# Kernel tuning notes

Measured on AMD Instinct MI355X. Metric: run time of the kernel, lower is better.

## Reference

```python
import jax, jax.numpy as jnp
import numpy as np

TP, TQ, B = 600, 60, 64          # passage len, question len, batch
H, H2, EMB = 256, 128, 344       # hidden, hidden//2, embed(300)+pos_tags(44)


def _lstm_cell(x, h, c, Wih, Whh, b):
    # PyTorch nn.LSTMCell math; b = b_ih + b_hh, gate order i,f,g,o
    g = x @ Wih.T + h @ Whh.T + b
    i, f, gg, o = jnp.split(g, 4, axis=-1)
    c2 = jax.nn.sigmoid(f) * c + jax.nn.sigmoid(i) * jnp.tanh(gg)
    return jax.nn.sigmoid(o) * jnp.tanh(c2), c2


def _pre_bilstm(x, mask, Wih, Whh, b):
    # Faithful quirk of the source: the cell's h output is DISCARDED;
    # c is masked and h = tanh(c).
    Bb = x.shape[1]
    init = (jnp.zeros((Bb, H2), x.dtype), jnp.zeros((Bb, H2), x.dtype))

    def step(carry, inp):
        h, c = carry
        xt, mt = inp
        _, c2 = _lstm_cell(xt, h, c, Wih, Whh, b)
        c2 = c2 * mt
        h2 = jnp.tanh(c2)
        return (h2, c2), h2

    _, Hf = jax.lax.scan(step, init, (x, mask))
    _, Hb = jax.lax.scan(step, init, (x[::-1], mask[::-1]))
    return jnp.concatenate([Hf, Hb[::-1]], axis=-1)  # [T,B,H]


def _match(Hp, Hq, mask, Wq, Wp, bp, Wh, Wa, ba, Wih, Whh, b):
    aq = Hq @ Wq.T           # [TQ,B,H] attend_question_for_passage (no bias)
    ap = Hp @ Wp.T + bp      # [TP,B,H] attend_passage_for_passage (precomputed)
    Bb = Hp.shape[1]
    init = (jnp.zeros((Bb, H2), Hp.dtype), jnp.zeros((Bb, H2), Hp.dtype))

    def step(carry, inp):
        h, c = carry
        apt, hpt, mt = inp
        g = jnp.tanh(aq + apt + h @ Wh.T)               # [TQ,B,H]
        alpha = jax.nn.softmax(g @ Wa.T + ba, axis=0)   # softmax over TQ, [TQ,B,1]
        wHq = jnp.einsum('tbo,tbh->bh', alpha, Hq)      # weighted question
        z = jnp.concatenate([hpt, wHq], axis=-1)        # [B,2H]
        h2, c2 = _lstm_cell(z, h, c, Wih, Whh, b)
        h2, c2 = h2 * mt, c2 * mt                       # mask applied to h and c
        return (h2, c2), h2

    _, Hf = jax.lax.scan(step, init, (ap, Hp, mask))
    _, Hb = jax.lax.scan(step, init, (ap[::-1], Hp[::-1], mask[::-1]))
    return jnp.concatenate([Hf, Hb[::-1]], axis=-1)  # [TP,B,H]


def setup_inputs() -> dict:
    key = jax.random.key(0)
    ks = iter(jax.random.split(key, 32))

    def w(shape, s=0.08):
        return jax.random.normal(next(ks), shape, jnp.float32) * s

    return {
        "passage": jax.random.normal(next(ks), (TP, B, EMB), jnp.float32),
        "question": jax.random.normal(next(ks), (TQ, B, EMB), jnp.float32),
        "mask_p": jnp.ones((TP, B, 1), jnp.float32),
        "mask_q": jnp.ones((TQ, B, 1), jnp.float32),
        "pre0_Wih": w((4 * H2, EMB)), "pre0_Whh": w((4 * H2, H2)), "pre0_b": w((4 * H2,)),
        "pre1_Wih": w((4 * H2, H)), "pre1_Whh": w((4 * H2, H2)), "pre1_b": w((4 * H2,)),
        "mq_Wq": w((H, H)), "mq_Wp": w((H, H)), "mq_bp": w((H,)),
        "mq_Wh": w((H, H2)), "mq_Wa": w((1, H)), "mq_ba": w((1,)),
        "mq_Wih": w((4 * H2, 2 * H)), "mq_Whh": w((4 * H2, H2)), "mq_b": w((4 * H2,)),
    }


def reference(passage, question, mask_p, mask_q,
              pre0_Wih, pre0_Whh, pre0_b,
              pre1_Wih, pre1_Whh, pre1_b,
              mq_Wq, mq_Wp, mq_bp, mq_Wh, mq_Wa, mq_ba,
              mq_Wih, mq_Whh, mq_b):
    # preprocessing layer 0 (shared LSTM for passage and question), dropout=0 eval
    Hp = _pre_bilstm(passage, mask_p, pre0_Wih, pre0_Whh, pre0_b)
    Hq = _pre_bilstm(question, mask_q, pre0_Wih, pre0_Whh, pre0_b)
    # preprocessing layer 1
    Hp = _pre_bilstm(Hp, mask_p, pre1_Wih, pre1_Whh, pre1_b)
    Hq = _pre_bilstm(Hq, mask_q, pre1_Wih, pre1_Whh, pre1_b)
    # passage Match-LSTM layer (bidirectional, question-attention per step)
    Hr = _match(Hp, Hq, mask_p, mq_Wq, mq_Wp, mq_bp, mq_Wh, mq_Wa, mq_ba,
                mq_Wih, mq_Whh, mq_b)
    return Hr  # [TP, B, H]
```

## Files before the change

### kernel.cpp

```cpp
#include <hip/hip_runtime.h>

typedef unsigned int u32;
typedef _Float16 f16x2 __attribute__((ext_vector_type(2)));

#define TP 600
#define TQ 60
#define BB 64
#define EMB 344
#define HH 256
#define H2 128
#define GG 512

__device__ __forceinline__ float exp2_fast(float x){
#if __has_builtin(__builtin_amdgcn_exp2f)
    return __builtin_amdgcn_exp2f(x);
#else
    return exp2f(x);
#endif
}
__device__ __forceinline__ float rcp_fast(float x){
#if __has_builtin(__builtin_amdgcn_rcpf)
    return __builtin_amdgcn_rcpf(x);
#else
    return 1.0f / x;
#endif
}
__device__ __forceinline__ float sigm_fast(float x){
    return rcp_fast(1.f + exp2_fast(-1.44269504f * x));
}
__device__ __forceinline__ float tanh_fast(float x){
    return 1.f - 2.f * rcp_fast(1.f + exp2_fast(2.88539008f * x));
}
__device__ __forceinline__ float dot2x(u32 w, u32 h, float acc){
    f16x2 wv = __builtin_bit_cast(f16x2, w);
    f16x2 hv = __builtin_bit_cast(f16x2, h);
    acc = fmaf((float)wv.x, (float)hv.x, acc);
    acc = fmaf((float)wv.y, (float)hv.y, acc);
    return acc;
}
__device__ __forceinline__ float dot2f(u32 w, u32 h, float acc){
#if __has_builtin(__builtin_amdgcn_fdot2)
    return __builtin_amdgcn_fdot2(__builtin_bit_cast(f16x2, w),
                                  __builtin_bit_cast(f16x2, h), acc, false);
#else
    return dot2x(w, h, acc);
#endif
}
__device__ __forceinline__ u32 pack2(float a, float b){
    f16x2 v; v.x = (_Float16)a; v.y = (_Float16)b;
    return __builtin_bit_cast(u32, v);
}
__device__ __forceinline__ u32 lane_bcast(u32 v, int l){
    return (u32)__builtin_amdgcn_readlane((int)v, l);
}
__device__ __forceinline__ void bar_lds(){
    asm volatile("s_waitcnt lgkmcnt(0)\n\ts_barrier" ::: "memory");
}

__global__ void prep_kernel(const float* __restrict__ pre0_Wih, const float* __restrict__ pre0_Whh,
                            const float* __restrict__ pre1_Wih, const float* __restrict__ pre1_Whh,
                            const float* __restrict__ Wq, const float* __restrict__ Wp,
                            const float* __restrict__ Whm,
                            const float* __restrict__ Whhm,
                            float* __restrict__ WT0, float* __restrict__ WT1,
                            float* __restrict__ WTq, float* __restrict__ WTp,
                            float* __restrict__ WTz, const float* __restrict__ Wihm,
                            u32* __restrict__ P0hh, u32* __restrict__ P1hh,
                            u32* __restrict__ PMhh, u32* __restrict__ PMwh)
{
    int g = blockIdx.x * blockDim.x + threadIdx.x;
    int gs = gridDim.x * blockDim.x;
    for (int idx = g; idx < 512*344; idx += gs) {
        int j = idx / 344, k = idx - j*344;
        WT0[((k>>2)*512 + j)*4 + (k&3)] = pre0_Wih[idx];
    }
    for (int idx = g; idx < 512*256; idx += gs) {
        int j = idx >> 8, k = idx & 255;
        WT1[((k>>2)*512 + j)*4 + (k&3)] = pre1_Wih[idx];
    }
    for (int idx = g; idx < 256*256; idx += gs) {
        int j = idx >> 8, k = idx & 255;
        WTq[((k>>2)*256 + j)*4 + (k&3)] = Wq[idx];
        WTp[((k>>2)*256 + j)*4 + (k&3)] = Wp[idx];
    }
    for (int idx = g; idx < 512*256; idx += gs) {
        int j = idx >> 8, k = idx & 255;
        WTz[((k>>2)*512 + j)*4 + (k&3)] = Wihm[j*512 + k];
    }
    for (int idx = g; idx < 64*512; idx += gs) {
        int k2 = idx >> 9, j = idx & 511;
        P0hh[idx] = pack2(pre0_Whh[j*128 + 2*k2], pre0_Whh[j*128 + 2*k2 + 1]);
        P1hh[idx] = pack2(pre1_Whh[j*128 + 2*k2], pre1_Whh[j*128 + 2*k2 + 1]);
        PMhh[idx] = pack2(Whhm[j*128 + 2*k2], Whhm[j*128 + 2*k2 + 1]);
    }
    for (int idx = g; idx < 64*256; idx += gs) {
        int k2 = idx >> 8, j = idx & 255;
        PMwh[idx] = pack2(Whm[j*128 + 2*k2], Whm[j*128 + 2*k2 + 1]);
    }
}

template<int K, int M>
__global__ __launch_bounds__(M)
void proj_kernel(const float* __restrict__ X0, const float* __restrict__ W0,
                 const float* __restrict__ b0, float* __restrict__ C0, int T0,
                 const float* __restrict__ X1, const float* __restrict__ W1,
                 const float* __restrict__ b1, float* __restrict__ C1)
{
    __shared__ float Xs[K*68];
    int t = blockIdx.x;
    const float* X; const float* W; const float* bias; float* C; int trow;
    if (t < T0) { X = X0; W = W0; bias = b0; C = C0; trow = t; }
    else        { X = X1; W = W1; bias = b1; C = C1; trow = t - T0; }
    int j = threadIdx.x;
    for (int b = 0; b < 64; ++b) {
        for (int k = j; k < K; k += M)
            Xs[k*68 + b] = X[(trow*64 + b)*K + k];
    }
    __syncthreads();
    float acc[64];
    float binit = bias ? bias[j] : 0.f;
    #pragma unroll
    for (int b = 0; b < 64; ++b) acc[b] = binit;
    const float4* W4 = (const float4*)W;
    for (int k4 = 0; k4 < K/4; ++k4) {
        float4 w4 = W4[k4*M + j];
        float wv[4] = {w4.x, w4.y, w4.z, w4.w};
        #pragma unroll
        for (int kk = 0; kk < 4; ++kk) {
            int k = 4*k4 + kk;
            #pragma unroll
            for (int b4 = 0; b4 < 16; ++b4) {
                float4 x4 = *((const float4*)&Xs[k*68 + 4*b4]);
                acc[4*b4+0] = fmaf(wv[kk], x4.x, acc[4*b4+0]);
                acc[4*b4+1] = fmaf(wv[kk], x4.y, acc[4*b4+1]);
                acc[4*b4+2] = fmaf(wv[kk], x4.z, acc[4*b4+2]);
                acc[4*b4+3] = fmaf(wv[kk], x4.w, acc[4*b4+3]);
            }
        }
    }
    for (int b = 0; b < 64; ++b)
        C[(trow*64 + b)*M + j] = acc[b];
}

__global__ __launch_bounds__(512)
void yq_kernel(const float* __restrict__ Hq1, const float* __restrict__ Wihm,
               float* __restrict__ Yq)
{
    __shared__ float Xs[256*68];
    int tq = blockIdx.x;
    int j = threadIdx.x;
    for (int b = 0; b < 64; ++b) {
        for (int k = j; k < 256; k += 512)
            Xs[k*68 + b] = Hq1[(tq*64 + b)*256 + k];
    }
    __syncthreads();
    float acc[64];
    #pragma unroll
    for (int b = 0; b < 64; ++b) acc[b] = 0.f;
    const float4* W4 = (const float4*)(Wihm + j*512 + 256);
    for (int k4 = 0; k4 < 64; ++k4) {
        float4 w4 = W4[k4];
        float wv[4] = {w4.x, w4.y, w4.z, w4.w};
        #pragma unroll
        for (int kk = 0; kk < 4; ++kk) {
            int k = 4*k4 + kk;
            #pragma unroll
            for (int b4 = 0; b4 < 16; ++b4) {
                float4 x4 = *((const float4*)&Xs[k*68 + 4*b4]);
                acc[4*b4+0] = fmaf(wv[kk], x4.x, acc[4*b4+0]);
                acc[4*b4+1] = fmaf(wv[kk], x4.y, acc[4*b4+1]);
                acc[4*b4+2] = fmaf(wv[kk], x4.z, acc[4*b4+2]);
                acc[4*b4+3] = fmaf(wv[kk], x4.w, acc[4*b4+3]);
            }
        }
    }
    for (int b = 0; b < 64; ++b)
        Yq[(tq*64 + b)*512 + j] = acc[b];
}

__global__ __launch_bounds__(128)
__attribute__((amdgpu_waves_per_eu(1, 1)))
void rec_pre_kernel(const float* __restrict__ Xp, const float* __restrict__ Xq,
                    const u32* __restrict__ Whh,
                    const float* __restrict__ mask_p, const float* __restrict__ mask_q,
                    float* __restrict__ Hp, float* __restrict__ Hq)
{
    int bid = blockIdx.x;
    int sub = bid & 127; int b = sub >> 1; int dir = sub & 1;
    const float* X; const float* mask; float* Hout; int T;
    if (bid < 128) { X = Xp; mask = mask_p; Hout = Hp; T = TP; }
    else           { X = Xq; mask = mask_q; Hout = Hq; T = TQ; }
    int j = threadIdx.x;
    int l = j & 63;
    __shared__ __align__(8) _Float16 hbuf[2][128];
    u32 wi[64], wf[64], wg[64];
    #pragma unroll
    for (int q = 0; q < 64; ++q) {
        wi[q] = Whh[q*512 +       j];
        wf[q] = Whh[q*512 + 128 + j];
        wg[q] = Whh[q*512 + 256 + j];
    }
    hbuf[0][j] = (_Float16)0.f;
    float c = 0.f;
    int t0 = dir ? (T-1) : 0;
    int t1i = (T > 1) ? (dir ? (T-2) : 1) : t0;
    float xi0 = X[(t0*64+b)*512 + j],       xf0 = X[(t0*64+b)*512 + 128 + j],
          xg0 = X[(t0*64+b)*512 + 256 + j], m0  = mask[t0*64+b];
    float xi1 = X[(t1i*64+b)*512 + j],       xf1 = X[(t1i*64+b)*512 + 128 + j],
          xg1 = X[(t1i*64+b)*512 + 256 + j], m1  = mask[t1i*64+b];
    bar_lds();
    int buf = 0;
    const u32* hb32 = (const u32*)hbuf;
    for (int s = 0; s < T; ++s) {
        int ti = dir ? (T-1-s) : s;
        int s2 = (s+2 < T) ? (s+2) : (T-1);
        int t2 = dir ? (T-1-s2) : s2;
        float xi2 = X[(t2*64+b)*512 + j],       xf2 = X[(t2*64+b)*512 + 128 + j],
              xg2 = X[(t2*64+b)*512 + 256 + j], m2  = mask[t2*64+b];
        u32 hp = hb32[buf*64 + l];
        float ai0 = xi0, ai1 = 0.f, af0 = xf0, af1 = 0.f, ag0 = xg0, ag1 = 0.f;
        #pragma unroll
        for (int q = 0; q < 64; q += 2) {
            u32 h0 = lane_bcast(hp, q), h1 = lane_bcast(hp, q+1);
            ai0 = dot2f(wi[q],   h0, ai0); af0 = dot2f(wf[q],   h0, af0); ag0 = dot2f(wg[q],   h0, ag0);
            ai1 = dot2f(wi[q+1], h1, ai1); af1 = dot2f(wf[q+1], h1, af1); ag1 = dot2f(wg[q+1], h1, ag1);
        }
        float gi = sigm_fast(ai0 + ai1);
        float gf = sigm_fast(af0 + af1);
        float gg = tanh_fast(ag0 + ag1);
        c = gf*c + gi*gg;
        c *= m0;
        float h = tanh_fast(c);
        hbuf[buf^1][j] = (_Float16)h;
        Hout[(ti*64 + b)*256 + dir*128 + j] = h;
        bar_lds();
        buf ^= 1;
        xi0=xi1; xf0=xf1; xg0=xg1; m0=m1;
        xi1=xi2; xf1=xf2; xg1=xg2; m1=m2;
    }
}

__global__ __launch_bounds__(512)
__attribute__((amdgpu_waves_per_eu(2, 2)))
void match_kernel(const float* __restrict__ ap,
                  const float* __restrict__ aqg,
                  const float* __restrict__ Zp,
                  const float* __restrict__ Yq,
                  const float* __restrict__ Wa,
                  const float* __restrict__ mask_p,
                  const u32* __restrict__ PMwh,
                  const u32* __restrict__ PMhh,
                  float* __restrict__ out)
{
    int bid = blockIdx.x; int b = bid >> 1; int dir = bid & 1;
    int tid = threadIdx.x;
    __shared__ __align__(16) u32 sumt16[160];
    __shared__ __align__(16) float gates[512];
    __shared__ __align__(16) _Float16 e16[64];

    int tq = tid >> 3, sb = tid & 7, l = tid & 63;

    u32 aqr[16];
    if (tq < 60) {
        #pragma unroll
        for (int i = 0; i < 16; ++i) {
            float2 a = *(const float2*)&aqg[(tq*64 + b)*256 + 32*sb + 2*i];
            aqr[i] = pack2(a.x, a.y);
        }
    } else {
        #pragma unroll
        for (int i = 0; i < 16; ++i) aqr[i] = 0u;
    }
    u32 wa_reg[16];
    #pragma unroll
    for (int i = 0; i < 16; ++i) {
        float2 w2 = *(const float2*)&Wa[32*sb + 2*i];
        wa_reg[i] = pack2(w2.x, w2.y);
    }
    u32 Yqr[32];
    #pragma unroll
    for (int r = 0; r < 30; ++r) {
        float y0 = Yq[((2*r  )*64 + b)*512 + tid];
        float y1 = Yq[((2*r+1)*64 + b)*512 + tid];
        Yqr[r] = pack2(y0, y1);
    }
    Yqr[30] = 0u; Yqr[31] = 0u;
    u32 whh[64];
    #pragma unroll
    for (int q = 0; q < 64; ++q) whh[q] = PMhh[q*512 + tid];
    u32 wh[64];
    {
        int jw = tid & 255;
        #pragma unroll
        for (int q = 0; q < 64; ++q) wh[q] = PMwh[q*256 + jw];
    }

    float c0 = 0.f, c1 = 0.f;
    u32 hp = 0u;
    int ti0 = dir ? (TP-1) : 0;
    float zp_c = Zp[(ti0*64 + b)*512 + tid];
    float ap_c = (tid < 256) ? ap[(ti0*64 + b)*256 + tid] : 0.f;
    float m_c  = mask_p[ti0*64 + b];
    int cls = tid >> 7;
    const u32 ONE2 = 0x3C003C00u;
    float h_out0 = 0.f, h_out1 = 0.f; int ti_prev = 0;
    bar_lds();

    const u32* e32 = (const u32*)e16;

    for (int s = 0; s < TP; ++s) {
        int ti = dir ? (TP-1-s) : s;
        int s1 = (s+1 < TP) ? (s+1) : s;
        int tn = dir ? (TP-1-s1) : s1;

        float w0 = 0.f, w1 = 0.f, w2a = 0.f, w3a = 0.f;
        if (tid < 256) {
            float s0 = ap_c, s1a = 0.f, s2 = 0.f, s3 = 0.f;
            #pragma unroll
            for (int q = 0; q < 64; q += 4) {
                u32 h0 = lane_bcast(hp, q),   u1 = lane_bcast(hp, q+1);
                u32 h2v = lane_bcast(hp, q+2), h3 = lane_bcast(hp, q+3);
                w0  = dot2f(whh[q],   h0,  w0);  s0  = dot2f(wh[q],   h0,  s0);
                w1  = dot2f(whh[q+1], u1,  w1);  s1a = dot2f(wh[q+1], u1,  s1a);
                w2a = dot2f(whh[q+2], h2v, w2a); s2  = dot2f(wh[q+2], h2v, s2);
                w3a = dot2f(whh[q+3], h3,  w3a); s3  = dot2f(wh[q+3], h3,  s3);
            }
            float st = (s0 + s1a) + (s2 + s3);
            float so = __shfl_xor(st, 1);
            if ((tid & 1) == 0) {
                int p = tid >> 1;
                sumt16[(p >> 4)*20 + (p & 15)] = pack2(st, so);
            }
        } else {
            #pragma unroll
            for (int q = 0; q < 64; q += 4) {
                u32 h0 = lane_bcast(hp, q),   u1 = lane_bcast(hp, q+1);
                u32 h2v = lane_bcast(hp, q+2), h3 = lane_bcast(hp, q+3);
                w0  = dot2f(whh[q],   h0,  w0);
                w1  = dot2f(whh[q+1], u1,  w1);
                w2a = dot2f(whh[q+2], h2v, w2a);
                w3a = dot2f(whh[q+3], h3,  w3a);
            }
        }
        float hwhh = (w0 + w1) + (w2a + w3a);
        bar_lds();

        if (s && tid < 64) {
            float2 hv; hv.x = h_out0; hv.y = h_out1;
            *(float2*)&out[(ti_prev*64 + b)*256 + dir*128 + 2*l] = hv;
        }
        float zp_n = Zp[(tn*64 + b)*512 + tid];
        float ap_n = (tid < 256) ? ap[(tn*64 + b)*256 + tid] : 0.f;
        float m_n  = mask_p[tn*64 + b];

        {
            const uint4* sv4 = (const uint4*)&sumt16[sb*20];
            uint4 sv0 = sv4[0], sv1 = sv4[1], sv2 = sv4[2], sv3 = sv4[3];
            u32 sa[16] = {sv0.x,sv0.y,sv0.z,sv0.w, sv1.x,sv1.y,sv1.z,sv1.w,
                          sv2.x,sv2.y,sv2.z,sv2.w, sv3.x,sv3.y,sv3.z,sv3.w};
            float p0 = 0.f, p1 = 0.f, p2 = 0.f, p3 = 0.f;
            #pragma unroll
            for (int i = 0; i < 16; ++i) {
                f16x2 sm = __builtin_bit_cast(f16x2, aqr[i]) +
                           __builtin_bit_cast(f16x2, sa[i]);
                f16x2 wv = __builtin_bit_cast(f16x2, wa_reg[i]);
                float t0 = tanh_fast((float)sm.x);
                float t1 = tanh_fast((float)sm.y);
                if (i & 1) { p2 = fmaf((float)wv.x, t0, p2); p3 = fmaf((float)wv.y, t1, p3); }
                else       { p0 = fmaf((float)wv.x, t0, p0); p1 = fmaf((float)wv.y, t1, p1); }
            }
            float part = (p0 + p1) + (p2 + p3);
            part += __shfl_xor(part, 1);
            part += __shfl_xor(part, 2);
            part += __shfl_xor(part, 4);
            float sc = fminf(9.f, fmaxf(-9.f, part));
            float e = exp2_fast(sc * 1.44269504f);
            if (tq >= 60) e = 0.f;
            if (sb == 0) e16[tq] = (_Float16)e;
        }
        bar_lds();

        {
            u32 ep = e32[l & 31];
            float y0 = 0.f, y1 = 0.f, S0 = 0.f, S1 = 0.f;
            #pragma unroll
            for (int r4 = 0; r4 < 8; ++r4) {
                u32 e0 = lane_bcast(ep, 4*r4+0), e1 = lane_bcast(ep, 4*r4+1);
                u32 e2 = lane_bcast(ep, 4*r4+2), e3 = lane_bcast(ep, 4*r4+3);
                y0 = dot2f(Yqr[4*r4+0], e0, y0); S0 = dot2f(ONE2, e0, S0);
                y1 = dot2f(Yqr[4*r4+1], e1, y1); S1 = dot2f(ONE2, e1, S1);
                y0 = dot2f(Yqr[4*r4+2], e2, y0); S0 = dot2f(ONE2, e2, S0);
                y1 = dot2f(Yqr[4*r4+3], e3, y1); S1 = dot2f(ONE2, e3, S1);
            }
            float rn = rcp_fast(S0 + S1);
            float g = zp_c + rn * (y0 + y1) + hwhh;
            gates[tid] = (cls == 2) ? tanh_fast(g) : sigm_fast(g);
        }
        bar_lds();

        {
            float2 gi2 = *(const float2*)&gates[      2*l];
            float2 gf2 = *(const float2*)&gates[128 + 2*l];
            float2 gg2 = *(const float2*)&gates[256 + 2*l];
            float2 go2 = *(const float2*)&gates[384 + 2*l];
            c0 = gf2.x*c0 + gi2.x*gg2.x;
            c1 = gf2.y*c1 + gi2.y*gg2.y;
            float h0 = go2.x * tanh_fast(c0);
            float h1 = go2.y * tanh_fast(c1);
            h0 *= m_c; h1 *= m_c; c0 *= m_c; c1 *= m_c;
            hp = pack2(h0, h1);
            h_out0 = h0; h_out1 = h1; ti_prev = ti;
        }
        zp_c = zp_n; ap_c = ap_n; m_c = m_n;
    }
    if (tid < 64) {
        float2 hv; hv.x = h_out0; hv.y = h_out1;
        *(float2*)&out[(ti_prev*64 + b)*256 + dir*128 + 2*l] = hv;
    }
}

#define O_BUFX   0UL
#define O_BUFXQ  19660800UL
#define O_HP0    21626880UL
#define O_HQ0    31457280UL
#define O_HP1    32440320UL
#define O_HQ1    42270720UL
#define O_WT0    43253760UL
#define O_WT1    43429888UL
#define O_WTQ    43560960UL
#define O_WTP    43626496UL
#define O_WTZ    43692032UL
#define O_P0HH   43823104UL
#define O_P1HH   43855872UL
#define O_PMHH   43888640UL
#define O_PMWH   43921408UL

extern "C" void kernel_launch(void* const* d_in, const int* in_sizes, int n_in,
                              void* d_out, int out_size, void* d_ws, size_t ws_size,
                              hipStream_t stream)
{
    const float* passage  = (const float*)d_in[0];
    const float* question = (const float*)d_in[1];
    const float* mask_p   = (const float*)d_in[2];
    const float* mask_q   = (const float*)d_in[3];
    const float* pre0_Wih = (const float*)d_in[4];
    const float* pre0_Whh = (const float*)d_in[5];
    const float* pre0_b   = (const float*)d_in[6];
    const float* pre1_Wih = (const float*)d_in[7];
    const float* pre1_Whh = (const float*)d_in[8];
    const float* pre1_b   = (const float*)d_in[9];
    const float* mq_Wq    = (const float*)d_in[10];
    const float* mq_Wp    = (const float*)d_in[11];
    const float* mq_bp    = (const float*)d_in[12];
    const float* mq_Wh    = (const float*)d_in[13];
    const float* mq_Wa    = (const float*)d_in[14];
    const float* mq_Wih   = (const float*)d_in[16];
    const float* mq_Whh   = (const float*)d_in[17];
    const float* mq_b     = (const float*)d_in[18];

    float* ws = (float*)d_ws;
    float* bufX  = ws + O_BUFX;
    float* bufXq = ws + O_BUFXQ;
    float* Hp0   = ws + O_HP0;
    float* Hq0   = ws + O_HQ0;
    float* Hp1   = ws + O_HP1;
    float* Hq1   = ws + O_HQ1;
    float* WT0   = ws + O_WT0;
    float* WT1   = ws + O_WT1;
    float* WTq   = ws + O_WTQ;
    float* WTp   = ws + O_WTP;
    float* WTz   = ws + O_WTZ;
    u32*   P0hh  = (u32*)(ws + O_P0HH);
    u32*   P1hh  = (u32*)(ws + O_P1HH);
    u32*   PMhh  = (u32*)(ws + O_PMHH);
    u32*   PMwh  = (u32*)(ws + O_PMWH);
    float* ap = Hp0;
    float* aq = Hq0;
    float* Zp = bufX;
    float* Yq = bufXq;

    prep_kernel<<<688, 256, 0, stream>>>(pre0_Wih, pre0_Whh, pre1_Wih, pre1_Whh,
                                         mq_Wq, mq_Wp, mq_Wh, mq_Whh,
                                         WT0, WT1, WTq, WTp, WTz, mq_Wih,
                                         P0hh, P1hh, PMhh, PMwh);
    proj_kernel<EMB, 512><<<660, 512, 0, stream>>>(passage, WT0, pre0_b, bufX, TP,
                                                   question, WT0, pre0_b, bufXq);
    rec_pre_kernel<<<256, 128, 0, stream>>>(bufX, bufXq, P0hh, mask_p, mask_q, Hp0, Hq0);
    proj_kernel<256, 512><<<660, 512, 0, stream>>>(Hp0, WT1, pre1_b, bufX, TP,
                                                   Hq0, WT1, pre1_b, bufXq);
    rec_pre_kernel<<<256, 128, 0, stream>>>(bufX, bufXq, P1hh, mask_p, mask_q, Hp1, Hq1);
    proj_kernel<256, 256><<<660, 256, 0, stream>>>(Hp1, WTp, mq_bp, ap, TP,
                                                   Hq1, WTq, nullptr, aq);
    proj_kernel<256, 512><<<600, 512, 0, stream>>>(Hp1, WTz, mq_b, Zp, TP,
                                                   nullptr, nullptr, nullptr, nullptr);
    yq_kernel<<<60, 512, 0, stream>>>(Hq1, mq_Wih, Yq);
    match_kernel<<<128, 512, 0, stream>>>(ap, aq, Zp, Yq, mq_Wa, mask_p,
                                          PMwh, PMhh, (float*)d_out);
}
```

Before: 3.820 ms.

## Split recurrent matvecs across more waves with warp-specialized partial sums

The pre-LSTM recurrence now uses 768 threads per block instead of 128. Six waves each compute half of the hidden-state dot product for the three gates, and a second group supplies the other half through shared memory. The match kernel grows to 1024 threads: one half computes the Whh gate matvec and the other computes the attention Wh projection. Both halves split the attention score and weighted-question reductions, and the partial results are combined in LDS. The aim is to shorten the serial per-step critical path by spreading register-resident weights and FLOPs over more waves, at the cost of extra barriers and LDS traffic per step.

```diff
diff --git a/kernel.cpp b/kernel.cpp
--- a/kernel.cpp
+++ b/kernel.cpp
@@ -55,6 +55,46 @@
 }
 __device__ __forceinline__ void bar_lds(){
     asm volatile("s_waitcnt lgkmcnt(0)\n\ts_barrier" ::: "memory");
+}
+
+__device__ __forceinline__ void attn_p2(int tq2, int sub, const u32* aqr,
+                                        const float* sumt_s, const float* wa_s,
+                                        _Float16* e16)
+{
+    float p0 = 0.f, p1 = 0.f;
+    #pragma unroll
+    for (int i = 0; i < 8; ++i) {
+        f16x2 av = __builtin_bit_cast(f16x2, aqr[i]);
+        float2 st = *(const float2*)&sumt_s[16*sub + 2*i];
+        float2 wv = *(const float2*)&wa_s[16*sub + 2*i];
+        p0 = fmaf(wv.x, tanh_fast((float)av.x + st.x), p0);
+        p1 = fmaf(wv.y, tanh_fast((float)av.y + st.y), p1);
+    }
+    float part = p0 + p1;
+    part += __shfl_xor(part, 1);
+    part += __shfl_xor(part, 2);
+    part += __shfl_xor(part, 4);
+    part += __shfl_xor(part, 8);
+    if (sub == 0 && tq2 < 60) {
+        float sc = fminf(9.f, fmaxf(-9.f, part));
+        e16[tq2] = (_Float16)exp2_fast(sc * 1.44269504f);
+    }
+}
+__device__ __forceinline__ void cell4(const float* gates, int l, float m,
+                                      float& c0, float& c1, u32& hp,
+                                      float& h0o, float& h1o)
+{
+    float2 gi2 = *(const float2*)&gates[      2*l];
+    float2 gf2 = *(const float2*)&gates[128 + 2*l];
+    float2 gg2 = *(const float2*)&gates[256 + 2*l];
+    float2 go2 = *(const float2*)&gates[384 + 2*l];
+    c0 = gf2.x*c0 + gi2.x*gg2.x;
+    c1 = gf2.y*c1 + gi2.y*gg2.y;
+    float h0 = go2.x * tanh_fast(c0);
+    float h1 = go2.y * tanh_fast(c1);
+    h0 *= m; h1 *= m; c0 *= m; c1 *= m;
+    hp = pack2(h0, h1);
+    h0o = h0; h1o = h1;
 }
 
 __global__ void prep_kernel(const float* __restrict__ pre0_Wih, const float* __restrict__ pre0_Whh,
@@ -178,70 +218,99 @@
         Yq[(tq*64 + b)*512 + j] = acc[b];
 }
 
-__global__ __launch_bounds__(128)
-__attribute__((amdgpu_waves_per_eu(1, 1)))
+__global__ __launch_bounds__(768)
 void rec_pre_kernel(const float* __restrict__ Xp, const float* __restrict__ Xq,
                     const u32* __restrict__ Whh,
                     const float* __restrict__ mask_p, const float* __restrict__ mask_q,
                     float* __restrict__ Hp, float* __restrict__ Hq)
 {
     int bid = blockIdx.x;
-    int sub = bid & 127; int b = sub >> 1; int dir = sub & 1;
+    int sb2 = bid & 127; int b = sb2 >> 1; int dir = sb2 & 1;
     const float* X; const float* mask; float* Hout; int T;
     if (bid < 128) { X = Xp; mask = mask_p; Hout = Hp; T = TP; }
     else           { X = Xq; mask = mask_q; Hout = Hq; T = TQ; }
-    int j = threadIdx.x;
-    int l = j & 63;
-    __shared__ __align__(8) _Float16 hbuf[2][128];
-    u32 wi[64], wf[64], wg[64];
-    #pragma unroll
-    for (int q = 0; q < 64; ++q) {
-        wi[q] = Whh[q*512 +       j];
-        wf[q] = Whh[q*512 + 128 + j];
-        wg[q] = Whh[q*512 + 256 + j];
-    }
-    hbuf[0][j] = (_Float16)0.f;
-    float c = 0.f;
+    int t = threadIdx.x;
+    int l = t & 63;
+    __shared__ float gates[384];
+    __shared__ float partG[384];
+    u32 hp = 0u;
+    float c0 = 0.f, c1 = 0.f;
     int t0 = dir ? (T-1) : 0;
     int t1i = (T > 1) ? (dir ? (T-2) : 1) : t0;
-    float xi0 = X[(t0*64+b)*512 + j],       xf0 = X[(t0*64+b)*512 + 128 + j],
-          xg0 = X[(t0*64+b)*512 + 256 + j], m0  = mask[t0*64+b];
-    float xi1 = X[(t1i*64+b)*512 + j],       xf1 = X[(t1i*64+b)*512 + 128 + j],
-          xg1 = X[(t1i*64+b)*512 + 256 + j], m1  = mask[t1i*64+b];
-    bar_lds();
-    int buf = 0;
-    const u32* hb32 = (const u32*)hbuf;
-    for (int s = 0; s < T; ++s) {
-        int ti = dir ? (T-1-s) : s;
-        int s2 = (s+2 < T) ? (s+2) : (T-1);
-        int t2 = dir ? (T-1-s2) : s2;
-        float xi2 = X[(t2*64+b)*512 + j],       xf2 = X[(t2*64+b)*512 + 128 + j],
-              xg2 = X[(t2*64+b)*512 + 256 + j], m2  = mask[t2*64+b];
-        u32 hp = hb32[buf*64 + l];
-        float ai0 = xi0, ai1 = 0.f, af0 = xf0, af1 = 0.f, ag0 = xg0, ag1 = 0.f;
-        #pragma unroll
-        for (int q = 0; q < 64; q += 2) {
-            u32 h0 = lane_bcast(hp, q), h1 = lane_bcast(hp, q+1);
-            ai0 = dot2f(wi[q],   h0, ai0); af0 = dot2f(wf[q],   h0, af0); ag0 = dot2f(wg[q],   h0, ag0);
-            ai1 = dot2f(wi[q+1], h1, ai1); af1 = dot2f(wf[q+1], h1, af1); ag1 = dot2f(wg[q+1], h1, ag1);
-        }
-        float gi = sigm_fast(ai0 + ai1);
-        float gf = sigm_fast(af0 + af1);
-        float gg = tanh_fast(ag0 + ag1);
-        c = gf*c + gi*gg;
-        c *= m0;
-        float h = tanh_fast(c);
-        hbuf[buf^1][j] = (_Float16)h;
-        Hout[(ti*64 + b)*256 + dir*128 + j] = h;
-        bar_lds();
-        buf ^= 1;
-        xi0=xi1; xf0=xf1; xg0=xg1; m0=m1;
-        xi1=xi2; xf1=xf2; xg1=xg2; m1=m2;
-    }
-}
-
-__global__ __launch_bounds__(512)
-__attribute__((amdgpu_waves_per_eu(2, 2)))
+    float m_c = mask[t0*64 + b];
+    float m_1 = mask[t1i*64 + b];
+
+    if (t < 384) {
+        int j = t;
+        u32 w[32];
+        #pragma unroll
+        for (int q = 0; q < 32; ++q) w[q] = Whh[q*512 + j];
+        float x_c = X[(t0*64 + b)*512 + j];
+        float x_1 = X[(t1i*64 + b)*512 + j];
+        float hd0, hd1;
+        for (int s = 0; s < T; ++s) {
+            int ti = dir ? (T-1-s) : s;
+            int s2 = (s+2 < T) ? (s+2) : (T-1);
+            int t2 = dir ? (T-1-s2) : s2;
+            float x_2 = X[(t2*64 + b)*512 + j];
+            float m_2 = mask[t2*64 + b];
+            float a0 = 0.f, a1 = 0.f;
+            #pragma unroll
+            for (int q = 0; q < 32; q += 2) {
+                a0 = dot2f(w[q],   lane_bcast(hp, q),   a0);
+                a1 = dot2f(w[q+1], lane_bcast(hp, q+1), a1);
+            }
+            bar_lds();
+            float g = x_c + (a0 + a1) + partG[j];
+            gates[j] = ((j >> 7) == 2) ? tanh_fast(g) : sigm_fast(g);
+            bar_lds();
+            {
+                float2 gi2 = *(const float2*)&gates[      2*l];
+                float2 gf2 = *(const float2*)&gates[128 + 2*l];
+                float2 gg2 = *(const float2*)&gates[256 + 2*l];
+                c0 = gf2.x*c0 + gi2.x*gg2.x;  c0 *= m_c;
+                c1 = gf2.y*c1 + gi2.y*gg2.y;  c1 *= m_c;
+                hd0 = tanh_fast(c0); hd1 = tanh_fast(c1);
+                hp = pack2(hd0, hd1);
+                if (t < 64) {
+                    float2 hv; hv.x = hd0; hv.y = hd1;
+                    *(float2*)&Hout[(ti*64 + b)*256 + dir*128 + 2*l] = hv;
+                }
+            }
+            x_c = x_1; x_1 = x_2; m_c = m_1; m_1 = m_2;
+        }
+    } else {
+        int j = t - 384;
+        u32 w[32];
+        #pragma unroll
+        for (int q = 0; q < 32; ++q) w[q] = Whh[(32 + q)*512 + j];
+        for (int s = 0; s < T; ++s) {
+            int s2 = (s+2 < T) ? (s+2) : (T-1);
+            int t2 = dir ? (T-1-s2) : s2;
+            float m_2 = mask[t2*64 + b];
+            float a0 = 0.f, a1 = 0.f;
+            #pragma unroll
+            for (int q = 0; q < 32; q += 2) {
+                a0 = dot2f(w[q],   lane_bcast(hp, 32 + q),     a0);
+                a1 = dot2f(w[q+1], lane_bcast(hp, 32 + q + 1), a1);
+            }
+            partG[j] = a0 + a1;
+            bar_lds();
+            bar_lds();
+            {
+                float2 gi2 = *(const float2*)&gates[      2*l];
+                float2 gf2 = *(const float2*)&gates[128 + 2*l];
+                float2 gg2 = *(const float2*)&gates[256 + 2*l];
+                c0 = gf2.x*c0 + gi2.x*gg2.x;  c0 *= m_c;
+                c1 = gf2.y*c1 + gi2.y*gg2.y;  c1 *= m_c;
+                hp = pack2(tanh_fast(c0), tanh_fast(c1));
+            }
+            m_c = m_1; m_1 = m_2;
+        }
+    }
+}
+
+__global__ __launch_bounds__(1024)
 void match_kernel(const float* __restrict__ ap,
                   const float* __restrict__ aqg,
                   const float* __restrict__ Zp,
@@ -253,169 +322,155 @@
                   float* __restrict__ out)
 {
     int bid = blockIdx.x; int b = bid >> 1; int dir = bid & 1;
-    int tid = threadIdx.x;
-    __shared__ __align__(16) u32 sumt16[160];
+    int t = threadIdx.x;
+    int l = t & 63;
+    int jj = t & 511;
+    int tq2 = t >> 4, sub = t & 15;
+    __shared__ __align__(16) float sumt_s[256];
+    __shared__ __align__(16) float wa_s[256];
     __shared__ __align__(16) float gates[512];
+    __shared__ __align__(16) float partY[512];
+    __shared__ __align__(16) float partS[512];
     __shared__ __align__(16) _Float16 e16[64];
 
-    int tq = tid >> 3, sb = tid & 7, l = tid & 63;
-
-    u32 aqr[16];
-    if (tq < 60) {
+    u32 aqr[8];
+    if (tq2 < 60) {
+        #pragma unroll
+        for (int i = 0; i < 8; ++i) {
+            float2 a = *(const float2*)&aqg[(tq2*64 + b)*256 + 16*sub + 2*i];
+            aqr[i] = pack2(a.x, a.y);
+        }
+    } else {
+        #pragma unroll
+        for (int i = 0; i < 8; ++i) aqr[i] = 0u;
+    }
+    u32 Yqr[16];
+    {
+        int pairbase = (t >> 9) * 16;
         #pragma unroll
         for (int i = 0; i < 16; ++i) {
-            float2 a = *(const float2*)&aqg[(tq*64 + b)*256 + 32*sb + 2*i];
-            aqr[i] = pack2(a.x, a.y);
-        }
-    } else {
-        #pragma unroll
-        for (int i = 0; i < 16; ++i) aqr[i] = 0u;
-    }
-    u32 wa_reg[16];
-    #pragma unroll
-    for (int i = 0; i < 16; ++i) {
-        float2 w2 = *(const float2*)&Wa[32*sb + 2*i];
-        wa_reg[i] = pack2(w2.x, w2.y);
-    }
-    u32 Yqr[32];
-    #pragma unroll
-    for (int r = 0; r < 30; ++r) {
-        float y0 = Yq[((2*r  )*64 + b)*512 + tid];
-        float y1 = Yq[((2*r+1)*64 + b)*512 + tid];
-        Yqr[r] = pack2(y0, y1);
-    }
-    Yqr[30] = 0u; Yqr[31] = 0u;
-    u32 whh[64];
-    #pragma unroll
-    for (int q = 0; q < 64; ++q) whh[q] = PMhh[q*512 + tid];
-    u32 wh[64];
-    {
-        int jw = tid & 255;
-        #pragma unroll
-        for (int q = 0; q < 64; ++q) wh[q] = PMwh[q*256 + jw];
-    }
-
+            int pr = pairbase + i;
+            int ta = 2*pr, tb = 2*pr + 1;
+            float ya = (ta < 60) ? Yq[(ta*64 + b)*512 + jj] : 0.f;
+            float yb = (tb < 60) ? Yq[(tb*64 + b)*512 + jj] : 0.f;
+            Yqr[i] = pack2(ya, yb);
+        }
+    }
+    if (t < 256) wa_s[t] = Wa[t];
+    if (t < 64)  e16[t] = (_Float16)0.f;
+    u32 hp = 0u;
     float c0 = 0.f, c1 = 0.f;
-    u32 hp = 0u;
     int ti0 = dir ? (TP-1) : 0;
-    float zp_c = Zp[(ti0*64 + b)*512 + tid];
-    float ap_c = (tid < 256) ? ap[(ti0*64 + b)*256 + tid] : 0.f;
-    float m_c  = mask_p[ti0*64 + b];
-    int cls = tid >> 7;
+    float m_c = mask_p[ti0*64 + b];
     const u32 ONE2 = 0x3C003C00u;
-    float h_out0 = 0.f, h_out1 = 0.f; int ti_prev = 0;
     bar_lds();
 
-    const u32* e32 = (const u32*)e16;
-
-    for (int s = 0; s < TP; ++s) {
-        int ti = dir ? (TP-1-s) : s;
-        int s1 = (s+1 < TP) ? (s+1) : s;
-        int tn = dir ? (TP-1-s1) : s1;
-
-        float w0 = 0.f, w1 = 0.f, w2a = 0.f, w3a = 0.f;
-        if (tid < 256) {
-            float s0 = ap_c, s1a = 0.f, s2 = 0.f, s3 = 0.f;
+    if (t < 512) {
+        u32 whh[64];
+        #pragma unroll
+        for (int q = 0; q < 64; ++q) whh[q] = PMhh[q*512 + jj];
+        float zp_c = Zp[(ti0*64 + b)*512 + jj];
+        float h_out0 = 0.f, h_out1 = 0.f; int ti_prev = 0;
+        for (int s = 0; s < TP; ++s) {
+            int ti = dir ? (TP-1-s) : s;
+            int s1 = (s+1 < TP) ? (s+1) : s;
+            int tn = dir ? (TP-1-s1) : s1;
+            float w0 = 0.f, w1 = 0.f, w2 = 0.f, w3 = 0.f;
             #pragma unroll
             for (int q = 0; q < 64; q += 4) {
-                u32 h0 = lane_bcast(hp, q),   u1 = lane_bcast(hp, q+1);
-                u32 h2v = lane_bcast(hp, q+2), h3 = lane_bcast(hp, q+3);
-                w0  = dot2f(whh[q],   h0,  w0);  s0  = dot2f(wh[q],   h0,  s0);
-                w1  = dot2f(whh[q+1], u1,  w1);  s1a = dot2f(wh[q+1], u1,  s1a);
-                w2a = dot2f(whh[q+2], h2v, w2a); s2  = dot2f(wh[q+2], h2v, s2);
-                w3a = dot2f(whh[q+3], h3,  w3a); s3  = dot2f(wh[q+3], h3,  s3);
-            }
-            float st = (s0 + s1a) + (s2 + s3);
-            float so = __shfl_xor(st, 1);
-            if ((tid & 1) == 0) {
-                int p = tid >> 1;
-                sumt16[(p >> 4)*20 + (p & 15)] = pack2(st, so);
-            }
-        } else {
-            #pragma unroll
-            for (int q = 0; q < 64; q += 4) {
-                u32 h0 = lane_bcast(hp, q),   u1 = lane_bcast(hp, q+1);
-                u32 h2v = lane_bcast(hp, q+2), h3 = lane_bcast(hp, q+3);
-                w0  = dot2f(whh[q],   h0,  w0);
-                w1  = dot2f(whh[q+1], u1,  w1);
-                w2a = dot2f(whh[q+2], h2v, w2a);
-                w3a = dot2f(whh[q+3], h3,  w3a);
-            }
-        }
-        float hwhh = (w0 + w1) + (w2a + w3a);
-        bar_lds();
-
-        if (s && tid < 64) {
+                w0 = dot2f(whh[q],   lane_bcast(hp, q),   w0);
+                w1 = dot2f(whh[q+1], lane_bcast(hp, q+1), w1);
+                w2 = dot2f(whh[q+2], lane_bcast(hp, q+2), w2);
+                w3 = dot2f(whh[q+3], lane_bcast(hp, q+3), w3);
+            }
+            float hwhh = (w0 + w1) + (w2 + w3);
+            bar_lds();
+            if (s && t < 64) {
+                float2 hv; hv.x = h_out0; hv.y = h_out1;
+                *(float2*)&out[(ti_prev*64 + b)*256 + dir*128 + 2*l] = hv;
+            }
+            float zp_n = Zp[(tn*64 + b)*512 + jj];
+            float m_n  = mask_p[tn*64 + b];
+            attn_p2(tq2, sub, aqr, sumt_s, wa_s, e16);
+            bar_lds();
+            float y0 = 0.f, y1 = 0.f, S0 = 0.f, S1 = 0.f;
+            {
+                u32 ep = ((const u32*)e16)[l & 31];
+                #pragma unroll
+                for (int r4 = 0; r4 < 4; ++r4) {
+                    u32 e0 = lane_bcast(ep, 4*r4+0), e1 = lane_bcast(ep, 4*r4+1);
+                    u32 e2 = lane_bcast(ep, 4*r4+2), e3 = lane_bcast(ep, 4*r4+3);
+                    y0 = dot2f(Yqr[4*r4+0], e0, y0); S0 = dot2f(ONE2, e0, S0);
+                    y1 = dot2f(Yqr[4*r4+1], e1, y1); S1 = dot2f(ONE2, e1, S1);
+                    y0 = dot2f(Yqr[4*r4+2], e2, y0); S0 = dot2f(ONE2, e2, S0);
+                    y1 = dot2f(Yqr[4*r4+3], e3, y1); S1 = dot2f(ONE2, e3, S1);
+                }
+            }
+            bar_lds();
+            {
+                float Sf = (S0 + S1) + partS[jj];
+                float yf = (y0 + y1) + partY[jj];
+                float rn = rcp_fast(Sf);
+                float g = zp_c + rn * yf + hwhh;
+                gates[jj] = ((jj >> 7) == 2) ? tanh_fast(g) : sigm_fast(g);
+            }
+            bar_lds();
+            cell4(gates, l, m_c, c0, c1, hp, h_out0, h_out1);
+            ti_prev = ti;
+            zp_c = zp_n; m_c = m_n;
+        }
+        if (t < 64) {
             float2 hv; hv.x = h_out0; hv.y = h_out1;
             *(float2*)&out[(ti_prev*64 + b)*256 + dir*128 + 2*l] = hv;
         }
-        float zp_n = Zp[(tn*64 + b)*512 + tid];
-        float ap_n = (tid < 256) ? ap[(tn*64 + b)*256 + tid] : 0.f;
-        float m_n  = mask_p[tn*64 + b];
-
-        {
-            const uint4* sv4 = (const uint4*)&sumt16[sb*20];
-            uint4 sv0 = sv4[0], sv1 = sv4[1], sv2 = sv4[2], sv3 = sv4[3];
-            u32 sa[16] = {sv0.x,sv0.y,sv0.z,sv0.w, sv1.x,sv1.y,sv1.z,sv1.w,
-                          sv2.x,sv2.y,sv2.z,sv2.w, sv3.x,sv3.y,sv3.z,sv3.w};
-            float p0 = 0.f, p1 = 0.f, p2 = 0.f, p3 = 0.f;
+    } else {
+        bool hasS = (t < 768);
+        u32 wh[64];
+        if (hasS) {
             #pragma unroll
-            for (int i = 0; i < 16; ++i) {
-                f16x2 sm = __builtin_bit_cast(f16x2, aqr[i]) +
-                           __builtin_bit_cast(f16x2, sa[i]);
-                f16x2 wv = __builtin_bit_cast(f16x2, wa_reg[i]);
-                float t0 = tanh_fast((float)sm.x);
-                float t1 = tanh_fast((float)sm.y);
-                if (i & 1) { p2 = fmaf((float)wv.x, t0, p2); p3 = fmaf((float)wv.y, t1, p3); }
-                else       { p0 = fmaf((float)wv.x, t0, p0); p1 = fmaf((float)wv.y, t1, p1); }
-            }
-            float part = (p0 + p1) + (p2 + p3);
-            part += __shfl_xor(part, 1);
-            part += __shfl_xor(part, 2);
-            part += __shfl_xor(part, 4);
-            float sc = fminf(9.f, fmaxf(-9.f, part));
-            float e = exp2_fast(sc * 1.44269504f);
-            if (tq >= 60) e = 0.f;
-            if (sb == 0) e16[tq] = (_Float16)e;
-        }
-        bar_lds();
-
-        {
-            u32 ep = e32[l & 31];
-            float y0 = 0.f, y1 = 0.f, S0 = 0.f, S1 = 0.f;
-            #pragma unroll
-            for (int r4 = 0; r4 < 8; ++r4) {
-                u32 e0 = lane_bcast(ep, 4*r4+0), e1 = lane_bcast(ep, 4*r4+1);
-                u32 e2 = lane_bcast(ep, 4*r4+2), e3 = lane_bcast(ep, 4*r4+3);
-                y0 = dot2f(Yqr[4*r4+0], e0, y0); S0 = dot2f(ONE2, e0, S0);
-                y1 = dot2f(Yqr[4*r4+1], e1, y1); S1 = dot2f(ONE2, e1, S1);
-                y0 = dot2f(Yqr[4*r4+2], e2, y0); S0 = dot2f(ONE2, e2, S0);
-                y1 = dot2f(Yqr[4*r4+3], e3, y1); S1 = dot2f(ONE2, e3, S1);
-            }
-            float rn = rcp_fast(S0 + S1);
-            float g = zp_c + rn * (y0 + y1) + hwhh;
-            gates[tid] = (cls == 2) ? tanh_fast(g) : sigm_fast(g);
-        }
-        bar_lds();
-
-        {
-            float2 gi2 = *(const float2*)&gates[      2*l];
-            float2 gf2 = *(const float2*)&gates[128 + 2*l];
-            float2 gg2 = *(const float2*)&gates[256 + 2*l];
-            float2 go2 = *(const float2*)&gates[384 + 2*l];
-            c0 = gf2.x*c0 + gi2.x*gg2.x;
-            c1 = gf2.y*c1 + gi2.y*gg2.y;
-            float h0 = go2.x * tanh_fast(c0);
-            float h1 = go2.y * tanh_fast(c1);
-            h0 *= m_c; h1 *= m_c; c0 *= m_c; c1 *= m_c;
-            hp = pack2(h0, h1);
-            h_out0 = h0; h_out1 = h1; ti_prev = ti;
-        }
-        zp_c = zp_n; ap_c = ap_n; m_c = m_n;
-    }
-    if (tid < 64) {
-        float2 hv; hv.x = h_out0; hv.y = h_out1;
-        *(float2*)&out[(ti_prev*64 + b)*256 + dir*128 + 2*l] = hv;
+            for (int q = 0; q < 64; ++q) wh[q] = PMwh[q*256 + jj];
+        }
+        float ap_c = hasS ? ap[(ti0*64 + b)*256 + jj] : 0.f;
+        float hd0, hd1;
+        for (int s = 0; s < TP; ++s) {
+            int s1 = (s+1 < TP) ? (s+1) : s;
+            int tn = dir ? (TP-1-s1) : s1;
+            if (hasS) {
+                float s0 = ap_c, s1a = 0.f, s2 = 0.f, s3 = 0.f;
+                #pragma unroll
+                for (int q = 0; q < 64; q += 4) {
+                    s0  = dot2f(wh[q],   lane_bcast(hp, q),   s0);
+                    s1a = dot2f(wh[q+1], lane_bcast(hp, q+1), s1a);
+                    s2  = dot2f(wh[q+2], lane_bcast(hp, q+2), s2);
+                    s3  = dot2f(wh[q+3], lane_bcast(hp, q+3), s3);
+                }
+                sumt_s[jj] = (s0 + s1a) + (s2 + s3);
+            }
+            bar_lds();
+            float ap_n = hasS ? ap[(tn*64 + b)*256 + jj] : 0.f;
+            float m_n  = mask_p[tn*64 + b];
+            attn_p2(tq2, sub, aqr, sumt_s, wa_s, e16);
+            bar_lds();
+            {
+                u32 ep = ((const u32*)e16)[l & 31];
+                float y0 = 0.f, y1 = 0.f, S0 = 0.f, S1 = 0.f;
+                #pragma unroll
+                for (int r4 = 0; r4 < 4; ++r4) {
+                    u32 e0 = lane_bcast(ep, 16+4*r4+0), e1 = lane_bcast(ep, 16+4*r4+1);
+                    u32 e2 = lane_bcast(ep, 16+4*r4+2), e3 = lane_bcast(ep, 16+4*r4+3);
+                    y0 = dot2f(Yqr[4*r4+0], e0, y0); S0 = dot2f(ONE2, e0, S0);
+                    y1 = dot2f(Yqr[4*r4+1], e1, y1); S1 = dot2f(ONE2, e1, S1);
+                    y0 = dot2f(Yqr[4*r4+2], e2, y0); S0 = dot2f(ONE2, e2, S0);
+                    y1 = dot2f(Yqr[4*r4+3], e3, y1); S1 = dot2f(ONE2, e3, S1);
+                }
+                partY[jj] = y0 + y1;
+                partS[jj] = S0 + S1;
+            }
+            bar_lds();
+            bar_lds();
+            cell4(gates, l, m_c, c0, c1, hp, hd0, hd1);
+            ap_c = ap_n; m_c = m_n;
+        }
     }
 }
 
@@ -485,15 +540,15 @@
                                          P0hh, P1hh, PMhh, PMwh);
     proj_kernel<EMB, 512><<<660, 512, 0, stream>>>(passage, WT0, pre0_b, bufX, TP,
                                                    question, WT0, pre0_b, bufXq);
-    rec_pre_kernel<<<256, 128, 0, stream>>>(bufX, bufXq, P0hh, mask_p, mask_q, Hp0, Hq0);
+    rec_pre_kernel<<<256, 768, 0, stream>>>(bufX, bufXq, P0hh, mask_p, mask_q, Hp0, Hq0);
     proj_kernel<256, 512><<<660, 512, 0, stream>>>(Hp0, WT1, pre1_b, bufX, TP,
                                                    Hq0, WT1, pre1_b, bufXq);
-    rec_pre_kernel<<<256, 128, 0, stream>>>(bufX, bufXq, P1hh, mask_p, mask_q, Hp1, Hq1);
+    rec_pre_kernel<<<256, 768, 0, stream>>>(bufX, bufXq, P1hh, mask_p, mask_q, Hp1, Hq1);
     proj_kernel<256, 256><<<660, 256, 0, stream>>>(Hp1, WTp, mq_bp, ap, TP,
                                                    Hq1, WTq, nullptr, aq);
     proj_kernel<256, 512><<<600, 512, 0, stream>>>(Hp1, WTz, mq_b, Zp, TP,
                                                    nullptr, nullptr, nullptr, nullptr);
     yq_kernel<<<60, 512, 0, stream>>>(Hq1, mq_Wih, Yq);
-    match_kernel<<<128, 512, 0, stream>>>(ap, aq, Zp, Yq, mq_Wa, mask_p,
-                                          PMwh, PMhh, (float*)d_out);
-}
+    match_kernel<<<128, 1024, 0, stream>>>(ap, aq, Zp, Yq, mq_Wa, mask_p,
+                                           PMwh, PMhh, (float*)d_out);
+}
```

Result: slower. 5.024 ms (+31.5%).
